# Performance work log

Hardware: AMD Instinct MI355X
Metric: run time of the kernel (lower is better)

Reference implementation:

```python
import jax, jax.numpy as jnp
import numpy as np

B, S, D, H, T = 128, 256, 256, 1024, 128  # batch, src_len, input/output_dim, hidden, target_len


def setup_inputs() -> dict:
    key = jax.random.key(0)
    ks = jax.random.split(key, 16)
    sc = 0.05

    def p(k, shape):
        return (jax.random.normal(k, shape, jnp.float32) * sc)

    return {
        "x": jax.random.normal(ks[0], (B, S, D), jnp.float32),
        "x_target": jax.random.normal(ks[1], (B, T, D), jnp.float32),
        # encoder bidirectional LSTM (1 layer): gates order i,f,g,o (PyTorch)
        "enc_Wih_f": p(ks[2], (4 * H, D)),  "enc_Whh_f": p(ks[3], (4 * H, H)), "enc_b_f": p(ks[4], (4 * H,)),
        "enc_Wih_b": p(ks[5], (4 * H, D)),  "enc_Whh_b": p(ks[6], (4 * H, H)), "enc_b_b": p(ks[7], (4 * H,)),
        # decoder bidirectional LSTM (1 layer)
        "dec_Wih_f": p(ks[8], (4 * H, D)),  "dec_Whh_f": p(ks[9], (4 * H, H)), "dec_b_f": p(ks[10], (4 * H,)),
        "dec_Wih_b": p(ks[11], (4 * H, D)), "dec_Whh_b": p(ks[12], (4 * H, H)), "dec_b_b": p(ks[13], (4 * H,)),
        # decoder head: Linear(2H -> D)
        "mlp_W": p(ks[14], (D, 2 * H)), "mlp_b": p(ks[15], (D,)),
    }


def lstm_cell(x, h, c, Wih, Whh, b):
    # x: [B, Din], h/c: [B, H]; PyTorch gate order i, f, g, o
    g = x @ Wih.T + h @ Whh.T + b
    i, f, gg, o = jnp.split(g, 4, axis=-1)
    c = jax.nn.sigmoid(f) * c + jax.nn.sigmoid(i) * jnp.tanh(gg)
    h = jax.nn.sigmoid(o) * jnp.tanh(c)
    return h, c


def run_dir(xs, Wih, Whh, b, reverse):
    # xs: [S, B, Din]; returns final (h, c) for one direction (zero init, like torch LSTM without h0)
    h0 = jnp.zeros((xs.shape[1], Whh.shape[1]), xs.dtype)
    c0 = jnp.zeros_like(h0)

    def step(carry, xt):
        h, c = lstm_cell(xt, *carry, Wih, Whh, b)
        return (h, c), None

    (h, c), _ = jax.lax.scan(step, (h0, c0), xs, reverse=reverse)
    return h, c


def reference(x, x_target, enc_Wih_f, enc_Whh_f, enc_b_f, enc_Wih_b, enc_Whh_b, enc_b_b,
              dec_Wih_f, dec_Whh_f, dec_b_f, dec_Wih_b, dec_Whh_b, dec_b_b, mlp_W, mlp_b):
    xs = jnp.transpose(x, (1, 0, 2))  # [S, B, D], time-major
    hf, cf = run_dir(xs, enc_Wih_f, enc_Whh_f, enc_b_f, reverse=False)
    hb, cb = run_dir(xs, enc_Wih_b, enc_Whh_b, enc_b_b, reverse=True)

    dec_in = x[:, -1, :]  # [B, D]

    def step(carry, _):
        hf, cf, hb, cb, inp = carry
        # bidirectional LSTM on a length-1 sequence: both directions see the same step
        hf2, cf2 = lstm_cell(inp, hf, cf, dec_Wih_f, dec_Whh_f, dec_b_f)
        hb2, cb2 = lstm_cell(inp, hb, cb, dec_Wih_b, dec_Whh_b, dec_b_b)
        out = jnp.concatenate([hf2, hb2], axis=-1) @ mlp_W.T + mlp_b  # [B, D]
        # teacher_forcing_ratio = 0.0 -> always feed model output back
        return (hf2, cf2, hb2, cb2, out), out

    _, outs = jax.lax.scan(step, (hf, cf, hb, cb, dec_in), None, length=T)
    return jnp.transpose(outs, (1, 0, 2))  # [B, T, D]
```

## Files before the change

### kernel.cpp

```cpp
#include <hip/hip_runtime.h>
#include <stdint.h>


typedef __attribute__((ext_vector_type(8))) short bfx8;
typedef __attribute__((ext_vector_type(4))) float f32x4;
typedef __attribute__((ext_vector_type(4))) unsigned short u16x4;
typedef unsigned short ushort_t;
typedef unsigned long long u64;

#define NWG 256
#define MFMA(a,b,c) __builtin_amdgcn_mfma_f32_16x16x32_bf16((a),(b),(c),0,0,0)
#define WAITVM(N) { asm volatile("s_waitcnt vmcnt(" #N ")" ::: "memory"); __builtin_amdgcn_sched_barrier(0); }
#define WAITLG(N) { asm volatile("s_waitcnt lgkmcnt(" #N ")" ::: "memory"); __builtin_amdgcn_sched_barrier(0); }
#define SBAR()    { __builtin_amdgcn_s_barrier(); __builtin_amdgcn_sched_barrier(0); }

__device__ __forceinline__ unsigned short f2bf(float f){
  unsigned u = __float_as_uint(f);
  u += 0x7FFFu + ((u >> 16) & 1u);
  return (unsigned short)(u >> 16);
}
__device__ __forceinline__ float bf2f(unsigned short h){
  return __uint_as_float(((unsigned)h) << 16);
}
__device__ __forceinline__ float sigm(float x){ return 1.f/(1.f + __expf(-x)); }
__device__ __forceinline__ float tanh_(float x){ return 1.f - 2.f/(__expf(2.f*x) + 1.f); }

__device__ __forceinline__ void stage16(const void* g, void* l){
  __builtin_amdgcn_global_load_lds((const __attribute__((address_space(1))) void*)g,
                                   (__attribute__((address_space(3))) void*)l,
                                   16, 0, 0);
}
__device__ __forceinline__ void stage16c(const void* g, void* l){
  __builtin_amdgcn_global_load_lds((const __attribute__((address_space(1))) void*)g,
                                   (__attribute__((address_space(3))) void*)l,
                                   16, 0, 0x11);
}

__device__ __forceinline__ bfx8 ld16c(const ushort_t* p){
  const u64* q = (const u64*)p;
  u64 a = __hip_atomic_load(q,     __ATOMIC_RELAXED, __HIP_MEMORY_SCOPE_AGENT);
  u64 b = __hip_atomic_load(q + 1, __ATOMIC_RELAXED, __HIP_MEMORY_SCOPE_AGENT);
  union { u64 u[2]; bfx8 v; } x; x.u[0] = a; x.u[1] = b; return x.v;
}
__device__ __forceinline__ void sth2(ushort_t* p, unsigned short v){
  __hip_atomic_store(p, v, __ATOMIC_RELAXED, __HIP_MEMORY_SCOPE_AGENT);
}

__device__ __forceinline__ void cvt2(const f32x4& a, const f32x4& b, bfx8& hi, bfx8& lo){
#pragma unroll
  for (int j = 0; j < 4; ++j){
    unsigned short h0 = f2bf(a[j]);
    unsigned short h1 = f2bf(b[j]);
    hi[j]   = (short)h0; lo[j]   = (short)f2bf(a[j] - bf2f(h0));
    hi[4+j] = (short)h1; lo[4+j] = (short)f2bf(b[j] - bf2f(h1));
  }
}

__device__ __forceinline__ void bar(unsigned* flags, int nflags, int me, unsigned gen){
  __syncthreads();
  if (threadIdx.x == 0)
    __hip_atomic_store(&flags[me], gen, __ATOMIC_RELAXED, __HIP_MEMORY_SCOPE_AGENT);
  if (threadIdx.x < 64){
    const int l = threadIdx.x;
    for (;;){
      unsigned mn = 0xFFFFFFFFu;
      for (int o = l; o < nflags; o += 64){
        unsigned v = __hip_atomic_load(&flags[o], __ATOMIC_RELAXED, __HIP_MEMORY_SCOPE_AGENT);
        mn = mn < v ? mn : v;
      }
      if (__all((int)(mn >= gen))) break;
      __builtin_amdgcn_s_sleep(1);
    }
  }
  __syncthreads();
}

struct WPre {
  const ushort_t* pj[8];
  ushort_t* ldsb[3];
  bool active;
};
__device__ __forceinline__ void wpre_issue(const WPre& w){
  if (!w.active) return;
#pragma unroll
  for (int bp = 0; bp < 3; ++bp)
#pragma unroll
    for (int j = 0; j < 8; ++j)
      stage16(w.pj[j] + bp*64, w.ldsb[bp] + j*512);
}
__device__ __forceinline__ void bar_pf(unsigned* flags, int nflags, int me,
                                       unsigned gen, const WPre& w, bool pf){
  WAITLG(0); WAITVM(0);
  SBAR();
  if (pf) wpre_issue(w);
  if (threadIdx.x == 192)
    __hip_atomic_store(&flags[me], gen, __ATOMIC_RELAXED, __HIP_MEMORY_SCOPE_AGENT);
  if ((threadIdx.x >> 6) == 3){
    const int l = threadIdx.x & 63;
    for (;;){
      unsigned mn = 0xFFFFFFFFu;
      for (int o = l; o < nflags; o += 64){
        unsigned v = __hip_atomic_load(&flags[o], __ATOMIC_RELAXED, __HIP_MEMORY_SCOPE_AGENT);
        mn = mn < v ? mn : v;
      }
      if (__all((int)(mn >= gen))) break;
      __builtin_amdgcn_s_sleep(1);
    }
  }
  SBAR();
}

struct Frags { bfx8 awh0, awh1, awl0, awl1, bh0, bh1, bl0, bl1; };

template<int ENC>
__device__ __forceinline__ void cell_step(
    const float*    __restrict__ Wih,
    const ushort_t* __restrict__ WhH,
    const ushort_t* __restrict__ WhL,
    const float*    __restrict__ bias,
    const float*    __restrict__ xsl,
    const ushort_t* __restrict__ iph,
    const ushort_t* __restrict__ ipl,
    const ushort_t* __restrict__ hh,
    const ushort_t* __restrict__ hl,
    ushort_t* __restrict__ outh, ushort_t* __restrict__ outl,
    float (&creg)[2][2],
    int r0, int n0, int b0, ushort_t* LDS)
{
  const int tid  = threadIdx.x;
  const int lane = tid & 63;
  const int wv   = tid >> 6;
  const int wm   = wv >> 1, wn = wv & 1;
  const int lr   = tid >> 3;
  const int lc   = tid & 7;
  const int cb   = lane >> 4;
  const int fr   = lane & 15;
  const int sc8  = lc ^ (lr & 7);
  const int sx   = fr & 7;
  const int rwa0 = wm*32 + fr, rwa1 = rwa0 + 16;
  const int rwb0 = wn*32 + fr, rwb1 = rwb0 + 16;

  const int ra = r0 + lr, rb = ra + 32;
  const float* wih0 = Wih + (size_t)((ra & 3)*1024 + (ra >> 2))*256 + sc8*8;
  const float* wih1 = Wih + (size_t)((rb & 3)*1024 + (rb >> 2))*256 + sc8*8;
  const float *xs0 = nullptr, *xs1 = nullptr;
  const ushort_t *ih0 = nullptr, *ih1 = nullptr, *il0 = nullptr, *il1 = nullptr;
  if (ENC){
    xs0 = xsl + (size_t)(b0 + lr)*65536 + sc8*8;
    xs1 = xs0 + (size_t)32*65536;
  } else {
    ih0 = iph + (size_t)(b0 + lr)*256 + sc8*8;  ih1 = ih0 + 32*256;
    il0 = ipl + (size_t)(b0 + lr)*256 + sc8*8;  il1 = il0 + 32*256;
  }

  const ushort_t* sb; size_t sstr; int srow0;
  if      (wv == 0){ sb = WhH; sstr = 1024; srow0 = r0; }
  else if (wv == 1){ sb = WhL; sstr = 1024; srow0 = r0; }
  else if (wv == 2){ sb = hh;  sstr = 2048; srow0 = b0; }
  else             { sb = hl;  sstr = 2048; srow0 = b0; }
  const int srw = lane >> 3;
  const int sg  = (lane & 7) ^ srw;
  const ushort_t* pj[8];
#pragma unroll
  for (int j = 0; j < 8; ++j)
    pj[j] = sb + (size_t)(srow0 + j*8 + srw)*sstr + sg*8;
  ushort_t* ldsb[3];
#pragma unroll
  for (int bp = 0; bp < 3; ++bp)
    ldsb[bp] = LDS + 16384 + bp*16384 + wv*4096;

  auto ISSUE = [&](int c, int bp){
    const int ko = (c - 4)*64;
    if (wv < 2){
#pragma unroll
      for (int j = 0; j < 8; ++j)
        stage16(pj[j] + ko, ldsb[bp] + j*512);
    } else {
#pragma unroll
      for (int j = 0; j < 8; ++j)
        stage16c(pj[j] + ko, ldsb[bp] + j*512);
    }
  };

  f32x4 acc[2][2] = {};
  auto rdf = [&](const ushort_t* buf, int ks, Frags& f){
    const int ga = (((ks << 2) + cb) ^ sx) << 3;
    f.awh0 = *(const bfx8*)(buf +         rwa0*64 + ga);
    f.awh1 = *(const bfx8*)(buf +         rwa1*64 + ga);
    f.awl0 = *(const bfx8*)(buf + 4096  + rwa0*64 + ga);
    f.awl1 = *(const bfx8*)(buf + 4096  + rwa1*64 + ga);
    f.bh0  = *(const bfx8*)(buf + 8192  + rwb0*64 + ga);
    f.bh1  = *(const bfx8*)(buf + 8192  + rwb1*64 + ga);
    f.bl0  = *(const bfx8*)(buf + 12288 + rwb0*64 + ga);
    f.bl1  = *(const bfx8*)(buf + 12288 + rwb1*64 + ga);
  };
  auto mm12 = [&](const Frags& f){
    acc[0][0] = MFMA(f.awh0, f.bh0, acc[0][0]);
    acc[0][0] = MFMA(f.awh0, f.bl0, acc[0][0]);
    acc[0][0] = MFMA(f.awl0, f.bh0, acc[0][0]);
    acc[0][1] = MFMA(f.awh0, f.bh1, acc[0][1]);
    acc[0][1] = MFMA(f.awh0, f.bl1, acc[0][1]);
    acc[0][1] = MFMA(f.awl0, f.bh1, acc[0][1]);
    acc[1][0] = MFMA(f.awh1, f.bh0, acc[1][0]);
    acc[1][0] = MFMA(f.awh1, f.bl0, acc[1][0]);
    acc[1][0] = MFMA(f.awl1, f.bh0, acc[1][0]);
    acc[1][1] = MFMA(f.awh1, f.bh1, acc[1][1]);
    acc[1][1] = MFMA(f.awh1, f.bl1, acc[1][1]);
    acc[1][1] = MFMA(f.awl1, f.bh1, acc[1][1]);
  };

  f32x4 rw0a, rw0b, rw1a, rw1b, rxa0, rxb0, rxa1, rxb1;
  bfx8 cwh0, cwh1, cwl0, cwl1, cah0, cah1, cal0, cal1;
  auto LOADRAW = [&](int kc){
    rw0a = *(const f32x4*)(wih0 + kc);  rw0b = *(const f32x4*)(wih0 + kc + 4);
    rw1a = *(const f32x4*)(wih1 + kc);  rw1b = *(const f32x4*)(wih1 + kc + 4);
    if (ENC){
      rxa0 = *(const f32x4*)(xs0 + kc); rxb0 = *(const f32x4*)(xs0 + kc + 4);
      rxa1 = *(const f32x4*)(xs1 + kc); rxb1 = *(const f32x4*)(xs1 + kc + 4);
    } else {
      cah0 = ld16c(ih0 + kc);  cah1 = ld16c(ih1 + kc);
      cal0 = ld16c(il0 + kc);  cal1 = ld16c(il1 + kc);
    }
  };
  auto CVT = [&](){
    cvt2(rw0a, rw0b, cwh0, cwl0);
    cvt2(rw1a, rw1b, cwh1, cwl1);
    if (ENC){ cvt2(rxa0, rxb0, cah0, cal0); cvt2(rxa1, rxb1, cah1, cal1); }
  };

  LOADRAW(0);
  if (wv >= 2){ ISSUE(4, 0); ISSUE(5, 1); ISSUE(6, 2); }
  CVT();

  for (int c = 0; c < 4; ++c){
    *(bfx8*)(LDS +         lr    *64 + lc*8) = cwh0;
    *(bfx8*)(LDS +        (lr+32)*64 + lc*8) = cwh1;
    *(bfx8*)(LDS + 4096 +  lr    *64 + lc*8) = cwl0;
    *(bfx8*)(LDS + 4096 + (lr+32)*64 + lc*8) = cwl1;
    *(bfx8*)(LDS + 8192 +  lr    *64 + lc*8) = cah0;
    *(bfx8*)(LDS + 8192 + (lr+32)*64 + lc*8) = cah1;
    *(bfx8*)(LDS + 12288 + lr    *64 + lc*8) = cal0;
    *(bfx8*)(LDS + 12288 +(lr+32)*64 + lc*8) = cal1;
    WAITLG(0); SBAR();
    if (c < 3) LOADRAW((c + 1)*64);
    Frags f0, f1;
    rdf(LDS, 0, f0);
    rdf(LDS, 1, f1);
    WAITLG(8);
    mm12(f0);
    WAITLG(0); SBAR();
    if (c < 3) CVT();
    mm12(f1);
  }

  int bi = 0;
  for (int i = 4; i <= 19; ++i){
    if (i < 18)      { WAITVM(16); }
    else if (i == 18){ WAITVM(8); }
    else             { WAITVM(0); }
    SBAR();
    const ushort_t* buf = LDS + 16384 + bi*16384;
    Frags f0, f1;
    rdf(buf, 0, f0);
    rdf(buf, 1, f1);
    WAITLG(8);
    mm12(f0);
    WAITLG(0); SBAR();
    if (i <= 16) ISSUE(i + 3, bi);
    mm12(f1);
    bi = (bi == 2) ? 0 : bi + 1;
  }

#pragma unroll
  for (int m = 0; m < 2; ++m){
    const int n = n0 + wm*8 + m*4 + cb;
    const float bi_ = bias[n];
    const float bf_ = bias[1024 + n];
    const float bg_ = bias[2048 + n];
    const float bo_ = bias[3072 + n];
#pragma unroll
    for (int nb = 0; nb < 2; ++nb){
      const int b = b0 + wn*32 + nb*16 + fr;
      float gi = acc[m][nb][0] + bi_;
      float gf = acc[m][nb][1] + bf_;
      float gg = acc[m][nb][2] + bg_;
      float go = acc[m][nb][3] + bo_;
      float c_new = sigm(gf)*creg[m][nb] + sigm(gi)*tanh_(gg);
      float h_new = sigm(go)*tanh_(c_new);
      creg[m][nb] = c_new;
      unsigned short hi = f2bf(h_new);
      sth2(&outh[(size_t)b*2048 + n], hi);
      sth2(&outl[(size_t)b*2048 + n], f2bf(h_new - bf2f(hi)));
    }
  }
}

__device__ __forceinline__ void mlp32(
    const ushort_t* __restrict__ hch, const ushort_t* __restrict__ hcl,
    const ushort_t* __restrict__ mWh, const ushort_t* __restrict__ mWl,
    const float* __restrict__ mb, float* __restrict__ dout,
    ushort_t* __restrict__ inph, ushort_t* __restrict__ inpl,
    int wg, int t, ushort_t* LDS)
{
  const int tid = threadIdx.x, lane = tid & 63, wv = tid >> 6;
  const int d0 = (wg >> 2)*32, b0 = (wg & 3)*32;
  const int kb = wv*512;
  const int srw2 = lane >> 2;
  const int pg   = lane & 3;

  const ushort_t* base[4] = { mWh, mWl, hch, hcl };
  const int rb0[4] = { d0, d0, b0, b0 };
  const ushort_t* sp[8];
#pragma unroll
  for (int j = 0; j < 8; ++j){
    const int p = j >> 1, sub = j & 1;
    const int rl = sub*16 + srw2;
    const int sr = (rl ^ (rl >> 2)) & 3;
    sp[j] = base[p] + (size_t)(rb0[p] + rl)*2048 + kb + ((pg ^ sr)*8);
  }
  ushort_t* lb[2] = { LDS + 16384 + wv*8192, LDS + 16384 + wv*8192 + 4096 };

  auto MISSUE = [&](int c){
    ushort_t* B = lb[c & 1];
    const int ko = c*32;
#pragma unroll
    for (int j = 0; j < 8; ++j){
      const int p = j >> 1, sub = j & 1;
      if (p < 2) stage16 (sp[j] + ko, B + p*1024 + sub*512 + lane*8);
      else       stage16c(sp[j] + ko, B + p*1024 + sub*512 + lane*8);
    }
  };
  MISSUE(0); MISSUE(1);

  f32x4 acc[2][2] = {};
  const int lg = lane >> 4;
  for (int c = 0; c < 16; ++c){
    if (c < 15) { WAITVM(8); } else { WAITVM(0); }
    const ushort_t* B = lb[c & 1];
    bfx8 wf[2][2], af[2][2];
#pragma unroll
    for (int m = 0; m < 2; ++m){
      const int rl = m*16 + (lane & 15);
      const int sr = (rl ^ (rl >> 2)) & 3;
      const int off = rl*32 + ((lg ^ sr)*8);
      wf[0][m] = *(const bfx8*)(B + off);
      wf[1][m] = *(const bfx8*)(B + 1024 + off);
      af[0][m] = *(const bfx8*)(B + 2048 + off);
      af[1][m] = *(const bfx8*)(B + 3072 + off);
    }
    WAITLG(0);
    if (c < 14) MISSUE(c + 2);
#pragma unroll
    for (int m = 0; m < 2; ++m)
#pragma unroll
      for (int n = 0; n < 2; ++n){
        acc[m][n] = MFMA(wf[0][m], af[0][n], acc[m][n]);
        acc[m][n] = MFMA(wf[0][m], af[1][n], acc[m][n]);
        acc[m][n] = MFMA(wf[1][m], af[0][n], acc[m][n]);
      }
  }

  float* PL = (float*)LDS;
#pragma unroll
  for (int m = 0; m < 2; ++m)
#pragma unroll
    for (int n = 0; n < 2; ++n)
#pragma unroll
      for (int r = 0; r < 4; ++r)
        PL[wv*1024 + (m*2 + n)*256 + r*64 + lane] = acc[m][n][r];
  __syncthreads();
  for (int o = tid; o < 1024; o += 256){
    float s = PL[o] + PL[1024 + o] + PL[2048 + o] + PL[3072 + o];
    const int m = o >> 9, n = (o >> 8) & 1, r = (o >> 6) & 3, l = o & 63;
    const int d = d0 + m*16 + (l >> 4)*4 + r;
    const int b = b0 + n*16 + (l & 15);
    s += mb[d];
    dout[((size_t)b*128 + t)*256 + d] = s;
    const unsigned short hv = f2bf(s);
    sth2(&inph[(size_t)b*256 + d], hv);
    sth2(&inpl[(size_t)b*256 + d], f2bf(s - bf2f(hv)));
  }
}

__device__ __forceinline__ void wg_decode(int wg, int& dir, int& r0, int& n0,
                                          int& b0, int& me){
  const int half = (wg >> 3) & 1;
  const int rgd  = (wg & 7) | ((wg >> 4) << 3);
  dir = rgd >> 6;
  const int rg = rgd & 63;
  r0 = rg * 64; n0 = rg * 16; b0 = half * 64;
  me = (rg << 1) | half;
}

__device__ __forceinline__ WPre make_wpre(const ushort_t* WhH, const ushort_t* WhL,
                                          int r0, ushort_t* LDS){
  const int tid = threadIdx.x, lane = tid & 63, wv = tid >> 6;
  const int srw = lane >> 3;
  const int sg  = (lane & 7) ^ srw;
  WPre w;
  w.active = (wv < 2);
  const ushort_t* sb = (wv == 1) ? WhL : WhH;
#pragma unroll
  for (int j = 0; j < 8; ++j)
    w.pj[j] = sb + (size_t)(r0 + j*8 + srw)*1024 + sg*8;
#pragma unroll
  for (int bp = 0; bp < 3; ++bp)
    w.ldsb[bp] = LDS + 16384 + bp*16384 + wv*4096;
  return w;
}

__global__ void __launch_bounds__(256) rnn_enc_kernel(
    const float* __restrict__ Wih_f, const float* __restrict__ b_f,
    const float* __restrict__ Wih_b, const float* __restrict__ b_b,
    const ushort_t* __restrict__ WhhH, const ushort_t* __restrict__ WhhL,
    const float* __restrict__ x,
    ushort_t* __restrict__ Hh, ushort_t* __restrict__ Hl,
    float* __restrict__ C, unsigned* flagsE)
{
  extern __shared__ ushort_t LDS[];
  int dir, r0, n0, b0, me;
  wg_decode(blockIdx.x, dir, r0, n0, b0, me);
  const float* Wih = dir ? Wih_b : Wih_f;
  const float* bia = dir ? b_b : b_f;
  const ushort_t* WhH = WhhH + (size_t)dir*4096*1024;
  const ushort_t* WhL = WhhL + (size_t)dir*4096*1024;
  unsigned* fl = flagsE + dir*128;
  const WPre wp = make_wpre(WhH, WhL, r0, LDS);

  float creg[2][2] = {{0.f, 0.f}, {0.f, 0.f}};
  wpre_issue(wp);
  for (int t = 0; t < 256; ++t){
    const int tt = dir ? (255 - t) : t;
    const int rp = t & 1;
    cell_step<1>(Wih, WhH, WhL, bia,
                 x + (size_t)tt*256, nullptr, nullptr,
                 Hh + (size_t)rp     *262144 + dir*1024,
                 Hl + (size_t)rp     *262144 + dir*1024,
                 Hh + (size_t)(rp^1) *262144 + dir*1024,
                 Hl + (size_t)(rp^1) *262144 + dir*1024,
                 creg, r0, n0, b0, LDS);
    bar_pf(fl, 128, me, (unsigned)(t + 1), wp, t < 255);
  }
  {
    const int lane = threadIdx.x & 63, wv = threadIdx.x >> 6;
    const int wm = wv >> 1, wn = wv & 1, cb = lane >> 4, fr = lane & 15;
    float* Cst = C + (size_t)dir*1024*128;
#pragma unroll
    for (int m = 0; m < 2; ++m)
#pragma unroll
      for (int nb = 0; nb < 2; ++nb){
        const int n = n0 + wm*8 + m*4 + cb;
        const int b = b0 + wn*32 + nb*16 + fr;
        Cst[n*128 + b] = creg[m][nb];
      }
  }
}

__global__ void __launch_bounds__(256) rnn_dec_kernel(
    const float* __restrict__ Wih_f, const float* __restrict__ b_f,
    const float* __restrict__ Wih_b, const float* __restrict__ b_b,
    const ushort_t* __restrict__ WhhH, const ushort_t* __restrict__ WhhL,
    const ushort_t* __restrict__ mWh, const ushort_t* __restrict__ mWl,
    const float* __restrict__ mb,
    ushort_t* __restrict__ Hh, ushort_t* __restrict__ Hl,
    float* __restrict__ C,
    ushort_t* __restrict__ inph, ushort_t* __restrict__ inpl,
    float* __restrict__ dout, unsigned* flagsD)
{
  extern __shared__ ushort_t LDS[];
  const int wg = blockIdx.x;
  int dir, r0, n0, b0, me;
  wg_decode(wg, dir, r0, n0, b0, me);
  const float* Wih = dir ? Wih_b : Wih_f;
  const float* bia = dir ? b_b : b_f;
  const ushort_t* WhH = WhhH + (size_t)dir*4096*1024;
  const ushort_t* WhL = WhhL + (size_t)dir*4096*1024;
  const WPre wp = make_wpre(WhH, WhL, r0, LDS);

  float creg[2][2];
  {
    const int lane = threadIdx.x & 63, wv = threadIdx.x >> 6;
    const int wm = wv >> 1, wn = wv & 1, cb = lane >> 4, fr = lane & 15;
    const float* Cst = C + (size_t)dir*1024*128;
#pragma unroll
    for (int m = 0; m < 2; ++m)
#pragma unroll
      for (int nb = 0; nb < 2; ++nb){
        const int n = n0 + wm*8 + m*4 + cb;
        const int b = b0 + wn*32 + nb*16 + fr;
        creg[m][nb] = Cst[n*128 + b];
      }
  }
  wpre_issue(wp);
  for (int t = 0; t < 128; ++t){
    const int rp = t & 1;
    cell_step<0>(Wih, WhH, WhL, bia,
                 nullptr, inph, inpl,
                 Hh + (size_t)rp     *262144 + dir*1024,
                 Hl + (size_t)rp     *262144 + dir*1024,
                 Hh + (size_t)(rp^1) *262144 + dir*1024,
                 Hl + (size_t)(rp^1) *262144 + dir*1024,
                 creg, r0, n0, b0, LDS);
    bar(flagsD, 256, wg, (unsigned)(2*t + 1));
    if (wg < 32)
      mlp32(Hh + (size_t)(rp^1)*262144, Hl + (size_t)(rp^1)*262144,
            mWh, mWl, mb, dout, inph, inpl, wg, t, LDS);
    bar_pf(flagsD, 256, wg, (unsigned)(2*t + 2), wp, t < 127);
  }
}

__global__ void k_wplanes(ushort_t* Hp, ushort_t* Lp,
                          const float* Whh_f, const float* Whh_b)
{
  const size_t N = 2ull*4096*1024;
  for (size_t i = (size_t)blockIdx.x*blockDim.x + threadIdx.x; i < N;
       i += (size_t)gridDim.x*blockDim.x){
    int dir = (int)(i >> 22);
    int r   = (int)((i >> 10) & 4095);
    int k   = (int)(i & 1023);
    int n = r >> 2, q = r & 3;
    const float* W = dir ? Whh_b : Whh_f;
    float v = W[(size_t)(q*1024 + n)*1024 + k];
    unsigned short h = f2bf(v);
    Hp[i] = h;
    Lp[i] = f2bf(v - bf2f(h));
  }
}

__global__ void k_init(ushort_t* Hh, ushort_t* Hl,
                       ushort_t* inph, ushort_t* inpl,
                       ushort_t* mWh, ushort_t* mWl,
                       const float* x, const float* mW, unsigned* cnt)
{
  const size_t N = 524288;
  for (size_t i = (size_t)blockIdx.x*blockDim.x + threadIdx.x; i < N;
       i += (size_t)gridDim.x*blockDim.x){
    Hh[i] = 0; Hl[i] = 0;
    float wv = mW[i];
    unsigned short wh = f2bf(wv);
    mWh[i] = wh;
    mWl[i] = f2bf(wv - bf2f(wh));
    if (i < 32768){
      int b = (int)(i >> 8), d = (int)(i & 255);
      float v = x[((size_t)b*256 + 255)*256 + d];
      unsigned short hi = f2bf(v);
      inph[i] = hi;
      inpl[i] = f2bf(v - bf2f(hi));
    }
    if (i < 2048) cnt[i] = 0;
  }
}

extern "C" void kernel_launch(void* const* d_in, const int* in_sizes, int n_in,
                              void* d_out, int out_size, void* d_ws, size_t ws_size,
                              hipStream_t stream)
{
  (void)in_sizes; (void)n_in; (void)out_size; (void)ws_size;
  const float* x      = (const float*)d_in[0];
  const float* eWih_f = (const float*)d_in[2];
  const float* eWhh_f = (const float*)d_in[3];
  const float* eb_f   = (const float*)d_in[4];
  const float* eWih_b = (const float*)d_in[5];
  const float* eWhh_b = (const float*)d_in[6];
  const float* eb_b   = (const float*)d_in[7];
  const float* dWih_f = (const float*)d_in[8];
  const float* dWhh_f = (const float*)d_in[9];
  const float* db_f   = (const float*)d_in[10];
  const float* dWih_b = (const float*)d_in[11];
  const float* dWhh_b = (const float*)d_in[12];
  const float* db_b   = (const float*)d_in[13];
  const float* mW     = (const float*)d_in[14];
  const float* mb     = (const float*)d_in[15];

  char* p = (char*)d_ws;
  size_t off = 0;
  unsigned* cnt   = (unsigned*)(p + off);  off += 8192;
  ushort_t* WhhEh = (ushort_t*)(p + off);  off += 16777216;
  ushort_t* WhhEl = (ushort_t*)(p + off);  off += 16777216;
  ushort_t* WhhDh = (ushort_t*)(p + off);  off += 16777216;
  ushort_t* WhhDl = (ushort_t*)(p + off);  off += 16777216;
  ushort_t* mWh   = (ushort_t*)(p + off);  off += 1048576;
  ushort_t* mWl   = (ushort_t*)(p + off);  off += 1048576;
  ushort_t* Hh    = (ushort_t*)(p + off);  off += 1048576;
  ushort_t* Hl    = (ushort_t*)(p + off);  off += 1048576;
  float*    C     = (float*)(p + off);     off += 1048576;
  ushort_t* inph  = (ushort_t*)(p + off);  off += 65536;
  ushort_t* inpl  = (ushort_t*)(p + off);  off += 65536;

  unsigned* flagsD = cnt;
  unsigned* flagsE = cnt + 256;

  hipFuncSetAttribute(reinterpret_cast<const void*>(rnn_enc_kernel),
                      hipFuncAttributeMaxDynamicSharedMemorySize, 131072);
  hipFuncSetAttribute(reinterpret_cast<const void*>(rnn_dec_kernel),
                      hipFuncAttributeMaxDynamicSharedMemorySize, 131072);

  k_init   <<<512, 256, 0, stream>>>(Hh, Hl, inph, inpl, mWh, mWl, x, mW, cnt);
  k_wplanes<<<2048, 256, 0, stream>>>(WhhEh, WhhEl, eWhh_f, eWhh_b);
  k_wplanes<<<2048, 256, 0, stream>>>(WhhDh, WhhDl, dWhh_f, dWhh_b);

  rnn_enc_kernel<<<NWG, 256, 131072, stream>>>(eWih_f, eb_f, eWih_b, eb_b,
                                               WhhEh, WhhEl, x, Hh, Hl, C, flagsE);
  rnn_dec_kernel<<<NWG, 256, 131072, stream>>>(dWih_f, db_f, dWih_b, db_b,
                                               WhhDh, WhhDl, mWh, mWl, mb,
                                               Hh, Hl, C, inph, inpl,
                                               (float*)d_out, flagsD);
}
```

Before: 10.22 ms.

## Split weight and hidden-state staging buffers and deepen async prefetch pipelines

The shared triple-buffered LDS staging ring for Whh and hidden state is replaced by separate rings: a double buffer for weight chunks (prefetched across the grid barrier) and a five-deep ring for the hidden state, with per-wave vmcnt waits adjusted to match. The input-projection phase now issues all four raw global loads up front instead of interleaving load and convert per chunk. The MLP head pipeline goes from two to four staged chunks. This aims to hide more global/L2 latency on the h-state loads that follow each barrier, at the cost of more LDS (raised to 144 KB) and higher register pressure from holding all four chunks of raw loads at once.

```diff
diff --git a/kernel.cpp b/kernel.cpp
--- a/kernel.cpp
+++ b/kernel.cpp
@@ -13,6 +13,7 @@
 #define WAITVM(N) { asm volatile("s_waitcnt vmcnt(" #N ")" ::: "memory"); __builtin_amdgcn_sched_barrier(0); }
 #define WAITLG(N) { asm volatile("s_waitcnt lgkmcnt(" #N ")" ::: "memory"); __builtin_amdgcn_sched_barrier(0); }
 #define SBAR()    { __builtin_amdgcn_s_barrier(); __builtin_amdgcn_sched_barrier(0); }
+#define SCHED0()  __builtin_amdgcn_sched_barrier(0)
 
 __device__ __forceinline__ unsigned short f2bf(float f){
   unsigned u = __float_as_uint(f);
@@ -77,13 +78,13 @@
 
 struct WPre {
   const ushort_t* pj[8];
-  ushort_t* ldsb[3];
+  ushort_t* ldsb[2];
   bool active;
 };
 __device__ __forceinline__ void wpre_issue(const WPre& w){
   if (!w.active) return;
 #pragma unroll
-  for (int bp = 0; bp < 3; ++bp)
+  for (int bp = 0; bp < 2; ++bp)
 #pragma unroll
     for (int j = 0; j < 8; ++j)
       stage16(w.pj[j] + bp*64, w.ldsb[bp] + j*512);
@@ -164,35 +165,33 @@
 #pragma unroll
   for (int j = 0; j < 8; ++j)
     pj[j] = sb + (size_t)(srow0 + j*8 + srw)*sstr + sg*8;
-  ushort_t* ldsb[3];
-#pragma unroll
-  for (int bp = 0; bp < 3; ++bp)
-    ldsb[bp] = LDS + 16384 + bp*16384 + wv*4096;
-
-  auto ISSUE = [&](int c, int bp){
+
+  auto ISSUE_W = [&](int c, int s){
     const int ko = (c - 4)*64;
-    if (wv < 2){
-#pragma unroll
-      for (int j = 0; j < 8; ++j)
-        stage16(pj[j] + ko, ldsb[bp] + j*512);
-    } else {
-#pragma unroll
-      for (int j = 0; j < 8; ++j)
-        stage16c(pj[j] + ko, ldsb[bp] + j*512);
-    }
+    ushort_t* d = LDS + 16384 + s*8192 + (wv & 1)*4096;
+#pragma unroll
+    for (int j = 0; j < 8; ++j)
+      stage16(pj[j] + ko, d + j*512);
   };
+  auto ISSUE_H = [&](int c, int s){
+    const int ko = (c - 4)*64;
+    ushort_t* d = LDS + 32768 + s*8192 + (wv & 1)*4096;
+#pragma unroll
+    for (int j = 0; j < 8; ++j)
+      stage16c(pj[j] + ko, d + j*512);
+  };
 
   f32x4 acc[2][2] = {};
-  auto rdf = [&](const ushort_t* buf, int ks, Frags& f){
+  auto rdf = [&](const ushort_t* wb, const ushort_t* ab, int ks, Frags& f){
     const int ga = (((ks << 2) + cb) ^ sx) << 3;
-    f.awh0 = *(const bfx8*)(buf +         rwa0*64 + ga);
-    f.awh1 = *(const bfx8*)(buf +         rwa1*64 + ga);
-    f.awl0 = *(const bfx8*)(buf + 4096  + rwa0*64 + ga);
-    f.awl1 = *(const bfx8*)(buf + 4096  + rwa1*64 + ga);
-    f.bh0  = *(const bfx8*)(buf + 8192  + rwb0*64 + ga);
-    f.bh1  = *(const bfx8*)(buf + 8192  + rwb1*64 + ga);
-    f.bl0  = *(const bfx8*)(buf + 12288 + rwb0*64 + ga);
-    f.bl1  = *(const bfx8*)(buf + 12288 + rwb1*64 + ga);
+    f.awh0 = *(const bfx8*)(wb +        rwa0*64 + ga);
+    f.awh1 = *(const bfx8*)(wb +        rwa1*64 + ga);
+    f.awl0 = *(const bfx8*)(wb + 4096 + rwa0*64 + ga);
+    f.awl1 = *(const bfx8*)(wb + 4096 + rwa1*64 + ga);
+    f.bh0  = *(const bfx8*)(ab +        rwb0*64 + ga);
+    f.bh1  = *(const bfx8*)(ab +        rwb1*64 + ga);
+    f.bl0  = *(const bfx8*)(ab + 4096 + rwb0*64 + ga);
+    f.bl1  = *(const bfx8*)(ab + 4096 + rwb1*64 + ga);
   };
   auto mm12 = [&](const Frags& f){
     acc[0][0] = MFMA(f.awh0, f.bh0, acc[0][0]);
@@ -209,66 +208,88 @@
     acc[1][1] = MFMA(f.awl1, f.bh1, acc[1][1]);
   };
 
-  f32x4 rw0a, rw0b, rw1a, rw1b, rxa0, rxb0, rxa1, rxb1;
-  bfx8 cwh0, cwh1, cwl0, cwl1, cah0, cah1, cal0, cal1;
-  auto LOADRAW = [&](int kc){
-    rw0a = *(const f32x4*)(wih0 + kc);  rw0b = *(const f32x4*)(wih0 + kc + 4);
-    rw1a = *(const f32x4*)(wih1 + kc);  rw1b = *(const f32x4*)(wih1 + kc + 4);
+  f32x4 rw[4][4];
+  f32x4 rx[4][4];
+  bfx8  di[4][4];
+#pragma unroll
+  for (int c = 0; c < 4; ++c){
+    const int kc = c*64;
+    rw[c][0] = *(const f32x4*)(wih0 + kc);  rw[c][1] = *(const f32x4*)(wih0 + kc + 4);
+    rw[c][2] = *(const f32x4*)(wih1 + kc);  rw[c][3] = *(const f32x4*)(wih1 + kc + 4);
     if (ENC){
-      rxa0 = *(const f32x4*)(xs0 + kc); rxb0 = *(const f32x4*)(xs0 + kc + 4);
-      rxa1 = *(const f32x4*)(xs1 + kc); rxb1 = *(const f32x4*)(xs1 + kc + 4);
+      rx[c][0] = *(const f32x4*)(xs0 + kc); rx[c][1] = *(const f32x4*)(xs0 + kc + 4);
+      rx[c][2] = *(const f32x4*)(xs1 + kc); rx[c][3] = *(const f32x4*)(xs1 + kc + 4);
     } else {
-      cah0 = ld16c(ih0 + kc);  cah1 = ld16c(ih1 + kc);
-      cal0 = ld16c(il0 + kc);  cal1 = ld16c(il1 + kc);
-    }
-  };
-  auto CVT = [&](){
-    cvt2(rw0a, rw0b, cwh0, cwl0);
-    cvt2(rw1a, rw1b, cwh1, cwl1);
-    if (ENC){ cvt2(rxa0, rxb0, cah0, cal0); cvt2(rxa1, rxb1, cah1, cal1); }
-  };
-
-  LOADRAW(0);
-  if (wv >= 2){ ISSUE(4, 0); ISSUE(5, 1); ISSUE(6, 2); }
-  CVT();
-
+      di[c][0] = ld16c(ih0 + kc);  di[c][1] = ld16c(ih1 + kc);
+      di[c][2] = ld16c(il0 + kc);  di[c][3] = ld16c(il1 + kc);
+    }
+  }
+  SCHED0();
+  if (wv >= 2){
+#pragma unroll
+    for (int s = 0; s < 5; ++s)
+      ISSUE_H(4 + s, s);
+  }
+  SCHED0();
+  bfx8 swh[4][2], swl[4][2], sah[4][2], sal[4][2];
+#pragma unroll
   for (int c = 0; c < 4; ++c){
-    *(bfx8*)(LDS +         lr    *64 + lc*8) = cwh0;
-    *(bfx8*)(LDS +        (lr+32)*64 + lc*8) = cwh1;
-    *(bfx8*)(LDS + 4096 +  lr    *64 + lc*8) = cwl0;
-    *(bfx8*)(LDS + 4096 + (lr+32)*64 + lc*8) = cwl1;
-    *(bfx8*)(LDS + 8192 +  lr    *64 + lc*8) = cah0;
-    *(bfx8*)(LDS + 8192 + (lr+32)*64 + lc*8) = cah1;
-    *(bfx8*)(LDS + 12288 + lr    *64 + lc*8) = cal0;
-    *(bfx8*)(LDS + 12288 +(lr+32)*64 + lc*8) = cal1;
+    cvt2(rw[c][0], rw[c][1], swh[c][0], swl[c][0]);
+    cvt2(rw[c][2], rw[c][3], swh[c][1], swl[c][1]);
+    if (ENC){
+      cvt2(rx[c][0], rx[c][1], sah[c][0], sal[c][0]);
+      cvt2(rx[c][2], rx[c][3], sah[c][1], sal[c][1]);
+    } else {
+      sah[c][0] = di[c][0]; sah[c][1] = di[c][1];
+      sal[c][0] = di[c][2]; sal[c][1] = di[c][3];
+    }
+  }
+
+#pragma unroll
+  for (int c = 0; c < 4; ++c){
+    *(bfx8*)(LDS +         lr    *64 + lc*8) = swh[c][0];
+    *(bfx8*)(LDS +        (lr+32)*64 + lc*8) = swh[c][1];
+    *(bfx8*)(LDS + 4096 +  lr    *64 + lc*8) = swl[c][0];
+    *(bfx8*)(LDS + 4096 + (lr+32)*64 + lc*8) = swl[c][1];
+    *(bfx8*)(LDS + 8192 +  lr    *64 + lc*8) = sah[c][0];
+    *(bfx8*)(LDS + 8192 + (lr+32)*64 + lc*8) = sah[c][1];
+    *(bfx8*)(LDS + 12288 + lr    *64 + lc*8) = sal[c][0];
+    *(bfx8*)(LDS + 12288 +(lr+32)*64 + lc*8) = sal[c][1];
     WAITLG(0); SBAR();
-    if (c < 3) LOADRAW((c + 1)*64);
     Frags f0, f1;
-    rdf(LDS, 0, f0);
-    rdf(LDS, 1, f1);
+    rdf(LDS, LDS + 8192, 0, f0);
+    rdf(LDS, LDS + 8192, 1, f1);
     WAITLG(8);
     mm12(f0);
     WAITLG(0); SBAR();
-    if (c < 3) CVT();
     mm12(f1);
   }
 
-  int bi = 0;
+  int hcs = 0, his = 0;
   for (int i = 4; i <= 19; ++i){
-    if (i < 18)      { WAITVM(16); }
-    else if (i == 18){ WAITVM(8); }
-    else             { WAITVM(0); }
+    if (wv < 2){
+      if (i <= 18) { WAITVM(8); } else { WAITVM(0); }
+    } else {
+      if      (i <= 15) { WAITVM(32); }
+      else if (i == 16) { WAITVM(24); }
+      else if (i == 17) { WAITVM(16); }
+      else if (i == 18) { WAITVM(8); }
+      else              { WAITVM(0); }
+    }
     SBAR();
-    const ushort_t* buf = LDS + 16384 + bi*16384;
+    const ushort_t* wb = LDS + 16384 + (i & 1)*8192;
+    const ushort_t* ab = LDS + 32768 + hcs*8192;
     Frags f0, f1;
-    rdf(buf, 0, f0);
-    rdf(buf, 1, f1);
+    rdf(wb, ab, 0, f0);
+    rdf(wb, ab, 1, f1);
     WAITLG(8);
     mm12(f0);
     WAITLG(0); SBAR();
-    if (i <= 16) ISSUE(i + 3, bi);
+    if (wv < 2){ if (i <= 17) ISSUE_W(i + 2, i & 1); }
+    else       { if (i <= 14) ISSUE_H(i + 5, his); }
     mm12(f1);
-    bi = (bi == 2) ? 0 : bi + 1;
+    hcs = (hcs == 4) ? 0 : hcs + 1;
+    his = (his == 4) ? 0 : his + 1;
   }
 
 #pragma unroll
@@ -318,10 +339,13 @@
     const int sr = (rl ^ (rl >> 2)) & 3;
     sp[j] = base[p] + (size_t)(rb0[p] + rl)*2048 + kb + ((pg ^ sr)*8);
   }
-  ushort_t* lb[2] = { LDS + 16384 + wv*8192, LDS + 16384 + wv*8192 + 4096 };
+  ushort_t* lb[4];
+#pragma unroll
+  for (int s = 0; s < 4; ++s)
+    lb[s] = LDS + 8192 + wv*16384 + s*4096;
 
   auto MISSUE = [&](int c){
-    ushort_t* B = lb[c & 1];
+    ushort_t* B = lb[c & 3];
     const int ko = c*32;
 #pragma unroll
     for (int j = 0; j < 8; ++j){
@@ -330,13 +354,16 @@
       else       stage16c(sp[j] + ko, B + p*1024 + sub*512 + lane*8);
     }
   };
-  MISSUE(0); MISSUE(1);
+  MISSUE(0); MISSUE(1); MISSUE(2); MISSUE(3);
 
   f32x4 acc[2][2] = {};
   const int lg = lane >> 4;
   for (int c = 0; c < 16; ++c){
-    if (c < 15) { WAITVM(8); } else { WAITVM(0); }
-    const ushort_t* B = lb[c & 1];
+    if      (c <= 12) { WAITVM(24); }
+    else if (c == 13) { WAITVM(16); }
+    else if (c == 14) { WAITVM(8); }
+    else              { WAITVM(0); }
+    const ushort_t* B = lb[c & 3];
     bfx8 wf[2][2], af[2][2];
 #pragma unroll
     for (int m = 0; m < 2; ++m){
@@ -349,7 +376,7 @@
       af[1][m] = *(const bfx8*)(B + 3072 + off);
     }
     WAITLG(0);
-    if (c < 14) MISSUE(c + 2);
+    if (c < 12) MISSUE(c + 4);
 #pragma unroll
     for (int m = 0; m < 2; ++m)
 #pragma unroll
@@ -404,8 +431,8 @@
   for (int j = 0; j < 8; ++j)
     w.pj[j] = sb + (size_t)(r0 + j*8 + srw)*1024 + sg*8;
 #pragma unroll
-  for (int bp = 0; bp < 3; ++bp)
-    w.ldsb[bp] = LDS + 16384 + bp*16384 + wv*4096;
+  for (int s = 0; s < 2; ++s)
+    w.ldsb[s] = LDS + 16384 + s*8192 + (wv & 1)*4096;
   return w;
 }
 
@@ -591,17 +618,17 @@
   unsigned* flagsE = cnt + 256;
 
   hipFuncSetAttribute(reinterpret_cast<const void*>(rnn_enc_kernel),
-                      hipFuncAttributeMaxDynamicSharedMemorySize, 131072);
+                      hipFuncAttributeMaxDynamicSharedMemorySize, 147456);
   hipFuncSetAttribute(reinterpret_cast<const void*>(rnn_dec_kernel),
-                      hipFuncAttributeMaxDynamicSharedMemorySize, 131072);
+                      hipFuncAttributeMaxDynamicSharedMemorySize, 147456);
 
   k_init   <<<512, 256, 0, stream>>>(Hh, Hl, inph, inpl, mWh, mWl, x, mW, cnt);
   k_wplanes<<<2048, 256, 0, stream>>>(WhhEh, WhhEl, eWhh_f, eWhh_b);
   k_wplanes<<<2048, 256, 0, stream>>>(WhhDh, WhhDl, dWhh_f, dWhh_b);
 
-  rnn_enc_kernel<<<NWG, 256, 131072, stream>>>(eWih_f, eb_f, eWih_b, eb_b,
+  rnn_enc_kernel<<<NWG, 256, 147456, stream>>>(eWih_f, eb_f, eWih_b, eb_b,
                                                WhhEh, WhhEl, x, Hh, Hl, C, flagsE);
-  rnn_dec_kernel<<<NWG, 256, 131072, stream>>>(dWih_f, db_f, dWih_b, db_b,
+  rnn_dec_kernel<<<NWG, 256, 147456, stream>>>(dWih_f, db_f, dWih_b, db_b,
                                                WhhDh, WhhDl, mWh, mWl, mb,
                                                Hh, Hl, C, inph, inpl,
                                                (float*)d_out, flagsD);
```

Measured after the change: 10.44 ms. +2.2%, slower.
